# Kernel optimization log

Hardware: AMD Instinct MI355X
Metric: run time of the kernel (lower is better)

## Reference

```python
import jax, jax.numpy as jnp
import numpy as np

N = 8192
IN_F = 128
OUT_F = 128


def setup_inputs() -> dict:
    key = jax.random.key(0)
    k1, k2, k3, k4 = jax.random.split(key, 4)
    h = jax.random.normal(k1, (N, IN_F), dtype=jnp.float32)
    pos = jax.random.normal(k2, (N, 1, 3), dtype=jnp.float32)
    # xavier_uniform-ish scale for params
    W = jax.random.uniform(k3, (IN_F, OUT_F), dtype=jnp.float32,
                           minval=-1.0, maxval=1.0) * (1.414 * np.sqrt(6.0 / (IN_F + OUT_F)))
    a = jax.random.uniform(k4, (2 * OUT_F + 3, 1), dtype=jnp.float32,
                           minval=-1.0, maxval=1.0) * (1.414 * np.sqrt(6.0 / (2 * OUT_F + 3 + 1)))
    return {"h": h, "pos": pos, "W": W, "a": a}


def reference(h, pos, W, a):
    # Wh: [N, F]
    Wh = h @ W
    F_ = Wh.shape[1]
    a1 = a[:F_, 0]          # weights on Wh[j] (the repeated / neighbor features)
    a2 = a[F_:2 * F_, 0]    # weights on Wh[i] (the repeat_interleaved / center features)
    a3 = a[2 * F_:, 0]      # weights on pos[i] - pos[j]
    p = pos.reshape(-1, 3)  # [N, 3]
    s_j = Wh @ a1           # [N]
    s_i = Wh @ a2           # [N]
    p_a = p @ a3            # [N]
    # e[i, j] = leaky_relu(Wh[j].a1 + Wh[i].a2 + (pos[i]-pos[j]).a3)
    e = jax.nn.leaky_relu(s_i[:, None] + s_j[None, :] + p_a[:, None] - p_a[None, :],
                          negative_slope=0.2)  # [N, N]
    attention = jax.nn.softmax(e, axis=1)
    # eval mode: dropout is identity
    h_prime = attention @ Wh  # [N, F]
    return jax.nn.elu(h_prime)
```

## Files before the change

### kernel.cpp

```cpp
#include <hip/hip_runtime.h>
#include <hip/hip_bf16.h>

#define N 8192
#define F 128
#define JC 16
#define JSLICE (N / JC)
#define RB 256

typedef __attribute__((ext_vector_type(4)))  float f32x4;
typedef __attribute__((ext_vector_type(16))) float f32x16;
typedef __attribute__((ext_vector_type(8)))  short short8;
typedef _Float16 f16x8 __attribute__((ext_vector_type(8)));

static __device__ __forceinline__ short bf16bits(float x) {
  __hip_bfloat16 b = __float2bfloat16(x);
  return *reinterpret_cast<short*>(&b);
}

__global__ __launch_bounds__(256) void k_gemm_cd(
    const float* __restrict__ h, const float* __restrict__ pos,
    const float* __restrict__ W, const float* __restrict__ a,
    unsigned short* __restrict__ WhTf, float* __restrict__ cArr,
    float* __restrict__ dArr)
{
  __shared__ float Ws[128 * 128];
  const int tid = threadIdx.x;
  const int r0  = blockIdx.x * 16;

  {
    f32x4* Ws4 = (f32x4*)Ws;
    const f32x4* Wg4 = (const f32x4*)W;
#pragma unroll
    for (int q = 0; q < 16; ++q) Ws4[q * 256 + tid] = Wg4[q * 256 + tid];
  }
  __syncthreads();

  const int rg  = tid >> 5;
  const int c32 = tid & 31;

  f32x4 acc0, acc1;
#pragma unroll
  for (int i = 0; i < 4; ++i) { acc0[i] = 0.0f; acc1[i] = 0.0f; }

  const f32x4* h40 = (const f32x4*)(h + (size_t)(r0 + rg * 2) * 128);
  const f32x4* h41 = (const f32x4*)(h + (size_t)(r0 + rg * 2 + 1) * 128);
  const f32x4* Ws4 = (const f32x4*)Ws;

#pragma unroll 4
  for (int k4 = 0; k4 < 32; ++k4) {
    f32x4 hv0 = h40[k4];
    f32x4 hv1 = h41[k4];
#pragma unroll
    for (int e = 0; e < 4; ++e) {
      f32x4 w = Ws4[(k4 * 4 + e) * 32 + c32];
      acc0 += hv0[e] * w;
      acc1 += hv1[e] * w;
    }
  }

  f32x4 a1v = *(const f32x4*)(a + c32 * 4);
  f32x4 a2v = *(const f32x4*)(a + 128 + c32 * 4);
#pragma unroll
  for (int rr = 0; rr < 2; ++rr) {
    f32x4 accR = rr ? acc1 : acc0;
    f32x4 t1 = accR * a1v;
    f32x4 t2 = accR * a2v;
    float s1 = t1[0] + t1[1] + t1[2] + t1[3];
    float s2 = t2[0] + t2[1] + t2[2] + t2[3];
#pragma unroll
    for (int m = 1; m < 32; m <<= 1) {
      s1 += __shfl_xor(s1, m);
      s2 += __shfl_xor(s2, m);
    }
    if (c32 == 0) {
      const int row = r0 + rg * 2 + rr;
      float pa = pos[row * 3 + 0] * a[256] + pos[row * 3 + 1] * a[257] +
                 pos[row * 3 + 2] * a[258];
      cArr[row] = s2 + pa;
      dArr[row] = s1 - pa;
    }
  }

  __syncthreads();
  float* tmp = Ws;
  {
    const int base = (rg * 2) * 132 + c32 * 4;
    *(f32x4*)&tmp[base]       = acc0;
    *(f32x4*)&tmp[base + 132] = acc1;
  }
  __syncthreads();
  {
    const int col  = tid >> 1;
    const int half = tid & 1;
    short8 o;
#pragma unroll
    for (int rr = 0; rr < 8; ++rr)
      o[rr] = bf16bits(tmp[(half * 8 + rr) * 132 + col]);
    *(short8*)(WhTf + (size_t)(r0 >> 4) * 2048 + col * 16 + half * 8) = o;
  }
}

__global__ __launch_bounds__(256) void k_dmax(
    const float* __restrict__ dArr, float* __restrict__ dmaxP)
{
  __shared__ float red[4];
  float m = -1e30f;
  const f32x4* d4 = (const f32x4*)dArr;
#pragma unroll
  for (int q = 0; q < 8; ++q) {
    f32x4 v = d4[threadIdx.x * 8 + q];
    m = fmaxf(m, fmaxf(fmaxf(v[0], v[1]), fmaxf(v[2], v[3])));
  }
#pragma unroll
  for (int s = 1; s < 64; s <<= 1) m = fmaxf(m, __shfl_xor(m, s));
  if ((threadIdx.x & 63) == 0) red[threadIdx.x >> 6] = m;
  __syncthreads();
  if (threadIdx.x == 0)
    dmaxP[0] = fmaxf(fmaxf(red[0], red[1]), fmaxf(red[2], red[3]));
}

__global__ __launch_bounds__(512, 4) void k_flash(
    const unsigned short* __restrict__ WhTf, const float* __restrict__ cArr,
    const float* __restrict__ dArr, const float* __restrict__ dmaxP,
    _Float16* __restrict__ pnum, float* __restrict__ pden)
{
  __shared__ __align__(16) float dS[JSLICE];

  const int tid = threadIdx.x;
  const int rb  = blockIdx.x & 31;
  const int jc  = blockIdx.x >> 5;
  const int r0  = rb * RB;

  const int w  = tid >> 6;
  const int l  = tid & 63;
  const int cl = l & 31;
  const int kh = l >> 5;

  if (tid < JSLICE / 4)
    ((f32x4*)dS)[tid] = ((const f32x4*)(dArr + (size_t)jc * JSLICE))[tid];
  __syncthreads();

  const float L2E = 1.44269504f;
  const float ci   = cArr[r0 + w * 32 + cl];
  const float dmax = dmaxP[0];
  float t0 = ci + dmax;
  const float negs = -L2E * fmaxf(t0, 0.2f * t0);

  f32x16 acc0, acc1, acc2, acc3;
#pragma unroll
  for (int i = 0; i < 16; ++i) { acc0[i] = 0; acc1[i] = 0; acc2[i] = 0; acc3[i] = 0; }
  float denA = 0.0f, denB = 0.0f;

  const unsigned short* bPtr =
      WhTf + (size_t)(jc * (JSLICE / 16)) * 2048 + cl * 16 + kh * 8;
  const float* dPtr = dS + kh * 8;

  short8 b0 = *(const short8*)(bPtr);
  short8 b1 = *(const short8*)(bPtr + 512);
  short8 b2 = *(const short8*)(bPtr + 1024);
  short8 b3 = *(const short8*)(bPtr + 1536);
  bPtr += 2048;

  const int iters = JSLICE / 16;
  for (int s = 0; s < iters; ++s) {
    short8 n0 = *(const short8*)(bPtr);
    short8 n1 = *(const short8*)(bPtr + 512);
    short8 n2 = *(const short8*)(bPtr + 1024);
    short8 n3 = *(const short8*)(bPtr + 1536);

    f32x4 dj0 = *(const f32x4*)(dPtr);
    f32x4 dj1 = *(const f32x4*)(dPtr + 4);

    short8 af;
#pragma unroll
    for (int e = 0; e < 8; ++e) {
      float dj = (e < 4) ? dj0[e] : dj1[e - 4];
      float t  = ci + dj;
      float lr = fmaxf(t, 0.2f * t);
      float pv = __builtin_amdgcn_exp2f(__builtin_fmaf(lr, L2E, negs));
      if (e & 1) denB += pv; else denA += pv;
      af[e] = bf16bits(pv);
    }

    __builtin_amdgcn_s_setprio(1);
    acc0 = __builtin_amdgcn_mfma_f32_32x32x16_bf16(af, b0, acc0, 0, 0, 0);
    acc1 = __builtin_amdgcn_mfma_f32_32x32x16_bf16(af, b1, acc1, 0, 0, 0);
    acc2 = __builtin_amdgcn_mfma_f32_32x32x16_bf16(af, b2, acc2, 0, 0, 0);
    acc3 = __builtin_amdgcn_mfma_f32_32x32x16_bf16(af, b3, acc3, 0, 0, 0);
    __builtin_amdgcn_s_setprio(0);

    b0 = n0; b1 = n1; b2 = n2; b3 = n3;
    bPtr += 2048; dPtr += 16;
  }

  float den = denA + denB;
  den += __shfl_xor(den, 32);

  {
    _Float16* base = pnum + (size_t)jc * N * F + (size_t)(r0 + w * 32) * 128;
#pragma unroll
    for (int reg = 0; reg < 16; ++reg) {
      const int row = (reg & 3) + 8 * (reg >> 2) + 4 * kh;
      _Float16* rp = base + row * 128 + cl;
      rp[0]  = (_Float16)acc0[reg];
      rp[32] = (_Float16)acc1[reg];
      rp[64] = (_Float16)acc2[reg];
      rp[96] = (_Float16)acc3[reg];
    }
    if (l < 32) pden[(size_t)jc * N + r0 + w * 32 + l] = den;
  }
}

__global__ __launch_bounds__(256) void k_final(
    const _Float16* __restrict__ pnum, const float* __restrict__ pden,
    float* __restrict__ out)
{
  const int g8 = blockIdx.x * 256 + threadIdx.x;
  const int row = g8 >> 4;
  float n[8];
#pragma unroll
  for (int i = 0; i < 8; ++i) n[i] = 0.0f;
  float dd = 0.0f;
#pragma unroll
  for (int c = 0; c < JC; ++c) {
    f16x8 hv = ((const f16x8*)(pnum + (size_t)c * N * F))[g8];
#pragma unroll
    for (int i = 0; i < 8; ++i) n[i] += (float)hv[i];
    dd += pden[(size_t)c * N + row];
  }
  const float inv = 1.0f / dd;
  f32x4 r0, r1;
#pragma unroll
  for (int i = 0; i < 4; ++i) { r0[i] = n[i] * inv; r1[i] = n[i + 4] * inv; }
#pragma unroll
  for (int i = 0; i < 4; ++i) {
    float x = r0[i];
    r0[i] = x > 0.0f ? x : (__builtin_amdgcn_exp2f(x * 1.44269504f) - 1.0f);
    float y = r1[i];
    r1[i] = y > 0.0f ? y : (__builtin_amdgcn_exp2f(y * 1.44269504f) - 1.0f);
  }
  ((f32x4*)out)[g8 * 2]     = r0;
  ((f32x4*)out)[g8 * 2 + 1] = r1;
}

extern "C" void kernel_launch(void* const* d_in, const int* in_sizes, int n_in,
                              void* d_out, int out_size, void* d_ws, size_t ws_size,
                              hipStream_t stream)
{
  const float* h   = (const float*)d_in[0];
  const float* pos = (const float*)d_in[1];
  const float* W   = (const float*)d_in[2];
  const float* a   = (const float*)d_in[3];
  float* out = (float*)d_out;

  char* ws = (char*)d_ws;
  unsigned short* WhTf = (unsigned short*)ws;
  float* cArr = (float*)(ws + (size_t)2 * 1024 * 1024);
  float* dArr = cArr + N;
  float* dmaxP = dArr + N;
  float* pden = dmaxP + 4;
  _Float16* pnum = (_Float16*)(pden + (size_t)JC * N);

  hipLaunchKernelGGL(k_gemm_cd, dim3(512), dim3(256), 0, stream,
                     h, pos, W, a, WhTf, cArr, dArr);
  hipLaunchKernelGGL(k_dmax, dim3(1), dim3(256), 0, stream, dArr, dmaxP);
  hipLaunchKernelGGL(k_flash, dim3((N / RB) * JC), dim3(512), 0, stream,
                     WhTf, cArr, dArr, dmaxP, pnum, pden);
  hipLaunchKernelGGL(k_final, dim3((N * F / 8) / 256), dim3(256), 0, stream,
                     pnum, pden, out);
}
```

Baseline: 109.3 us.

## Fuse dmax into flash kernel, double rows per wave, prescale by log2e

Removes the separate single-block dmax kernel; each flash block now recomputes the global max of d from all N values itself. Blocks shrink to 4 waves, and each wave handles 64 rows instead of 32, so every B fragment loaded feeds 8 MFMAs instead of 4. Scores are prescaled by log2(e) in the GEMM kernel, which removes an FMA per exponential. The inner loop is split into chunks of 8 with a periodic s_barrier to keep the waves in step. The cost is higher register pressure from 128 accumulator floats per lane, and every block now redundantly reads the whole 32 KB d array.

```diff
diff --git a/kernel.cpp b/kernel.cpp
--- a/kernel.cpp
+++ b/kernel.cpp
@@ -5,7 +5,6 @@
 #define F 128
 #define JC 16
 #define JSLICE (N / JC)
-#define RB 256
 
 typedef __attribute__((ext_vector_type(4)))  float f32x4;
 typedef __attribute__((ext_vector_type(16))) float f32x16;
@@ -20,8 +19,8 @@
 __global__ __launch_bounds__(256) void k_gemm_cd(
     const float* __restrict__ h, const float* __restrict__ pos,
     const float* __restrict__ W, const float* __restrict__ a,
-    unsigned short* __restrict__ WhTf, float* __restrict__ cArr,
-    float* __restrict__ dArr)
+    unsigned short* __restrict__ WhTf, float* __restrict__ cArrL,
+    float* __restrict__ dArrL)
 {
   __shared__ float Ws[128 * 128];
   const int tid = threadIdx.x;
@@ -76,8 +75,9 @@
       const int row = r0 + rg * 2 + rr;
       float pa = pos[row * 3 + 0] * a[256] + pos[row * 3 + 1] * a[257] +
                  pos[row * 3 + 2] * a[258];
-      cArr[row] = s2 + pa;
-      dArr[row] = s1 - pa;
+      const float L2E = 1.44269504f;
+      cArrL[row] = (s2 + pa) * L2E;
+      dArrL[row] = (s1 - pa) * L2E;
     }
   }
 
@@ -100,56 +100,55 @@
   }
 }
 
-__global__ __launch_bounds__(256) void k_dmax(
-    const float* __restrict__ dArr, float* __restrict__ dmaxP)
-{
-  __shared__ float red[4];
-  float m = -1e30f;
-  const f32x4* d4 = (const f32x4*)dArr;
-#pragma unroll
-  for (int q = 0; q < 8; ++q) {
-    f32x4 v = d4[threadIdx.x * 8 + q];
-    m = fmaxf(m, fmaxf(fmaxf(v[0], v[1]), fmaxf(v[2], v[3])));
-  }
-#pragma unroll
-  for (int s = 1; s < 64; s <<= 1) m = fmaxf(m, __shfl_xor(m, s));
-  if ((threadIdx.x & 63) == 0) red[threadIdx.x >> 6] = m;
-  __syncthreads();
-  if (threadIdx.x == 0)
-    dmaxP[0] = fmaxf(fmaxf(red[0], red[1]), fmaxf(red[2], red[3]));
-}
-
-__global__ __launch_bounds__(512, 4) void k_flash(
-    const unsigned short* __restrict__ WhTf, const float* __restrict__ cArr,
-    const float* __restrict__ dArr, const float* __restrict__ dmaxP,
-    _Float16* __restrict__ pnum, float* __restrict__ pden)
+__global__ __launch_bounds__(256, 2) void k_flash(
+    const unsigned short* __restrict__ WhTf, const float* __restrict__ cArrL,
+    const float* __restrict__ dArrL, _Float16* __restrict__ pnum,
+    float* __restrict__ pden)
 {
   __shared__ __align__(16) float dS[JSLICE];
+  __shared__ float dmS[4];
 
   const int tid = threadIdx.x;
   const int rb  = blockIdx.x & 31;
   const int jc  = blockIdx.x >> 5;
-  const int r0  = rb * RB;
+  const int r0  = rb * 256;
 
   const int w  = tid >> 6;
   const int l  = tid & 63;
   const int cl = l & 31;
   const int kh = l >> 5;
 
-  if (tid < JSLICE / 4)
-    ((f32x4*)dS)[tid] = ((const f32x4*)(dArr + (size_t)jc * JSLICE))[tid];
-  __syncthreads();
-
-  const float L2E = 1.44269504f;
-  const float ci   = cArr[r0 + w * 32 + cl];
-  const float dmax = dmaxP[0];
-  float t0 = ci + dmax;
-  const float negs = -L2E * fmaxf(t0, 0.2f * t0);
-
-  f32x16 acc0, acc1, acc2, acc3;
-#pragma unroll
-  for (int i = 0; i < 16; ++i) { acc0[i] = 0; acc1[i] = 0; acc2[i] = 0; acc3[i] = 0; }
-  float denA = 0.0f, denB = 0.0f;
+  {
+    float m = -1e30f;
+    const f32x4* dg = (const f32x4*)dArrL;
+#pragma unroll
+    for (int q = 0; q < 8; ++q) {
+      f32x4 v = dg[tid * 8 + q];
+      m = fmaxf(fmaxf(fmaxf(v[0], v[1]), fmaxf(v[2], v[3])), m);
+    }
+#pragma unroll
+    for (int s = 1; s < 64; s <<= 1) m = fmaxf(m, __shfl_xor(m, s));
+    if (l == 0) dmS[w] = m;
+    if (tid < JSLICE / 4)
+      ((f32x4*)dS)[tid] = ((const f32x4*)(dArrL + (size_t)jc * JSLICE))[tid];
+  }
+  __syncthreads();
+  const float dmax = fmaxf(fmaxf(dmS[0], dmS[1]), fmaxf(dmS[2], dmS[3]));
+
+  const float c0 = cArrL[r0 + w * 64 + cl];
+  const float c1 = cArrL[r0 + w * 64 + 32 + cl];
+  const float t0m = c0 + dmax, t1m = c1 + dmax;
+  const float negs0 = -fmaxf(t0m, 0.2f * t0m);
+  const float negs1 = -fmaxf(t1m, 0.2f * t1m);
+
+  f32x16 acc[2][4];
+#pragma unroll
+  for (int R = 0; R < 2; ++R)
+#pragma unroll
+    for (int G = 0; G < 4; ++G)
+#pragma unroll
+      for (int i = 0; i < 16; ++i) acc[R][G][i] = 0.0f;
+  float den0 = 0.0f, den1 = 0.0f;
 
   const unsigned short* bPtr =
       WhTf + (size_t)(jc * (JSLICE / 16)) * 2048 + cl * 16 + kh * 8;
@@ -161,53 +160,71 @@
   short8 b3 = *(const short8*)(bPtr + 1536);
   bPtr += 2048;
 
-  const int iters = JSLICE / 16;
-  for (int s = 0; s < iters; ++s) {
-    short8 n0 = *(const short8*)(bPtr);
-    short8 n1 = *(const short8*)(bPtr + 512);
-    short8 n2 = *(const short8*)(bPtr + 1024);
-    short8 n3 = *(const short8*)(bPtr + 1536);
-
-    f32x4 dj0 = *(const f32x4*)(dPtr);
-    f32x4 dj1 = *(const f32x4*)(dPtr + 4);
-
-    short8 af;
-#pragma unroll
-    for (int e = 0; e < 8; ++e) {
-      float dj = (e < 4) ? dj0[e] : dj1[e - 4];
-      float t  = ci + dj;
-      float lr = fmaxf(t, 0.2f * t);
-      float pv = __builtin_amdgcn_exp2f(__builtin_fmaf(lr, L2E, negs));
-      if (e & 1) denB += pv; else denA += pv;
-      af[e] = bf16bits(pv);
-    }
-
-    __builtin_amdgcn_s_setprio(1);
-    acc0 = __builtin_amdgcn_mfma_f32_32x32x16_bf16(af, b0, acc0, 0, 0, 0);
-    acc1 = __builtin_amdgcn_mfma_f32_32x32x16_bf16(af, b1, acc1, 0, 0, 0);
-    acc2 = __builtin_amdgcn_mfma_f32_32x32x16_bf16(af, b2, acc2, 0, 0, 0);
-    acc3 = __builtin_amdgcn_mfma_f32_32x32x16_bf16(af, b3, acc3, 0, 0, 0);
-    __builtin_amdgcn_s_setprio(0);
-
-    b0 = n0; b1 = n1; b2 = n2; b3 = n3;
-    bPtr += 2048; dPtr += 16;
-  }
-
-  float den = denA + denB;
-  den += __shfl_xor(den, 32);
-
-  {
-    _Float16* base = pnum + (size_t)jc * N * F + (size_t)(r0 + w * 32) * 128;
+  for (int oc = 0; oc < 4; ++oc) {
+#pragma unroll
+    for (int ic = 0; ic < 8; ++ic) {
+      short8 n0 = *(const short8*)(bPtr);
+      short8 n1 = *(const short8*)(bPtr + 512);
+      short8 n2 = *(const short8*)(bPtr + 1024);
+      short8 n3 = *(const short8*)(bPtr + 1536);
+
+      f32x4 dj0 = *(const f32x4*)(dPtr);
+      f32x4 dj1 = *(const f32x4*)(dPtr + 4);
+
+      short8 af0, af1;
+#pragma unroll
+      for (int e = 0; e < 8; ++e) {
+        float dj = (e < 4) ? dj0[e] : dj1[e - 4];
+        float t  = c0 + dj;
+        float pv = __builtin_amdgcn_exp2f(fmaxf(t, 0.2f * t) + negs0);
+        den0 += pv;
+        af0[e] = bf16bits(pv);
+        float u  = c1 + dj;
+        float qv = __builtin_amdgcn_exp2f(fmaxf(u, 0.2f * u) + negs1);
+        den1 += qv;
+        af1[e] = bf16bits(qv);
+      }
+
+      __builtin_amdgcn_s_setprio(1);
+      acc[0][0] = __builtin_amdgcn_mfma_f32_32x32x16_bf16(af0, b0, acc[0][0], 0, 0, 0);
+      acc[1][0] = __builtin_amdgcn_mfma_f32_32x32x16_bf16(af1, b0, acc[1][0], 0, 0, 0);
+      acc[0][1] = __builtin_amdgcn_mfma_f32_32x32x16_bf16(af0, b1, acc[0][1], 0, 0, 0);
+      acc[1][1] = __builtin_amdgcn_mfma_f32_32x32x16_bf16(af1, b1, acc[1][1], 0, 0, 0);
+      acc[0][2] = __builtin_amdgcn_mfma_f32_32x32x16_bf16(af0, b2, acc[0][2], 0, 0, 0);
+      acc[1][2] = __builtin_amdgcn_mfma_f32_32x32x16_bf16(af1, b2, acc[1][2], 0, 0, 0);
+      acc[0][3] = __builtin_amdgcn_mfma_f32_32x32x16_bf16(af0, b3, acc[0][3], 0, 0, 0);
+      acc[1][3] = __builtin_amdgcn_mfma_f32_32x32x16_bf16(af1, b3, acc[1][3], 0, 0, 0);
+      __builtin_amdgcn_s_setprio(0);
+
+      b0 = n0; b1 = n1; b2 = n2; b3 = n3;
+      bPtr += 2048; dPtr += 16;
+    }
+    __builtin_amdgcn_s_barrier();
+  }
+
+  den0 += __shfl_xor(den0, 32);
+  den1 += __shfl_xor(den1, 32);
+
+  {
+    _Float16* base = pnum + (size_t)jc * N * F + (size_t)(r0 + w * 64) * 128;
 #pragma unroll
     for (int reg = 0; reg < 16; ++reg) {
       const int row = (reg & 3) + 8 * (reg >> 2) + 4 * kh;
-      _Float16* rp = base + row * 128 + cl;
-      rp[0]  = (_Float16)acc0[reg];
-      rp[32] = (_Float16)acc1[reg];
-      rp[64] = (_Float16)acc2[reg];
-      rp[96] = (_Float16)acc3[reg];
-    }
-    if (l < 32) pden[(size_t)jc * N + r0 + w * 32 + l] = den;
+      _Float16* rp0 = base + row * 128 + cl;
+      rp0[0]  = (_Float16)acc[0][0][reg];
+      rp0[32] = (_Float16)acc[0][1][reg];
+      rp0[64] = (_Float16)acc[0][2][reg];
+      rp0[96] = (_Float16)acc[0][3][reg];
+      _Float16* rp1 = base + (32 + row) * 128 + cl;
+      rp1[0]  = (_Float16)acc[1][0][reg];
+      rp1[32] = (_Float16)acc[1][1][reg];
+      rp1[64] = (_Float16)acc[1][2][reg];
+      rp1[96] = (_Float16)acc[1][3][reg];
+    }
+    if (l < 32) {
+      pden[(size_t)jc * N + r0 + w * 64 + l]      = den0;
+      pden[(size_t)jc * N + r0 + w * 64 + 32 + l] = den1;
+    }
   }
 }
 
@@ -255,17 +272,15 @@
 
   char* ws = (char*)d_ws;
   unsigned short* WhTf = (unsigned short*)ws;
-  float* cArr = (float*)(ws + (size_t)2 * 1024 * 1024);
-  float* dArr = cArr + N;
-  float* dmaxP = dArr + N;
-  float* pden = dmaxP + 4;
+  float* cArrL = (float*)(ws + (size_t)2 * 1024 * 1024);
+  float* dArrL = cArrL + N;
+  float* pden = dArrL + N;
   _Float16* pnum = (_Float16*)(pden + (size_t)JC * N);
 
   hipLaunchKernelGGL(k_gemm_cd, dim3(512), dim3(256), 0, stream,
-                     h, pos, W, a, WhTf, cArr, dArr);
-  hipLaunchKernelGGL(k_dmax, dim3(1), dim3(256), 0, stream, dArr, dmaxP);
-  hipLaunchKernelGGL(k_flash, dim3((N / RB) * JC), dim3(512), 0, stream,
-                     WhTf, cArr, dArr, dmaxP, pnum, pden);
+                     h, pos, W, a, WhTf, cArrL, dArrL);
+  hipLaunchKernelGGL(k_flash, dim3(32 * JC), dim3(256), 0, stream,
+                     WhTf, cArrL, dArrL, pnum, pden);
   hipLaunchKernelGGL(k_final, dim3((N * F / 8) / 256), dim3(256), 0, stream,
                      pnum, pden, out);
 }
```

After: 104.6 us. 4.3% less time.
